# Kernel tuning notes

Hardware: AMD Instinct MI355X
Metric: run time of the kernel (lower is better)

The kernel has to match this reference:

```python
import jax, jax.numpy as jnp
import numpy as np

B = 8192         # graphs per batch
NPG = 39         # nodes per graph (from 4560 = 40*(105+9))
N = B * NPG      # total nodes
DEG = 8          # avg degree
E = N * DEG      # total edges
NEG_SLOPE = 0.2


def _glorot(key, shape):
    fan = sum(shape) if len(shape) > 1 else shape[0] + 1
    s = jnp.sqrt(6.0 / fan)
    return jax.random.uniform(key, shape, jnp.float32, -s, s)


def setup_inputs() -> dict:
    key = jax.random.key(0)
    ks = jax.random.split(key, 32)
    x = jax.random.normal(ks[0], (N, 1), jnp.float32)
    # edges constrained within each graph
    epg = NPG * DEG
    off = jnp.repeat(jnp.arange(B, dtype=jnp.int64) * NPG, epg)
    src = jax.random.randint(ks[1], (B * epg,), 0, NPG, jnp.int64) + off
    dst = jax.random.randint(ks[2], (B * epg,), 0, NPG, jnp.int64) + off
    edge_index = jnp.stack([src, dst], 0)
    batch_ids = jnp.repeat(jnp.arange(B, dtype=jnp.int64), NPG)
    dims = [(1, 8), (8, 64), (64, 32), (32, 9)]
    p = {}
    ki = 3
    for li, (fi, fo) in enumerate(dims, 1):
        p[f'W{li}'] = _glorot(ks[ki], (fi, fo)); ki += 1
        p[f'as{li}'] = _glorot(ks[ki], (fo,)); ki += 1
        p[f'ad{li}'] = _glorot(ks[ki], (fo,)); ki += 1
        p[f'b{li}'] = jnp.zeros((fo,), jnp.float32)
    p['lw1'] = _glorot(ks[ki], (4560, 1024)); ki += 1
    p['lb1'] = jnp.zeros((1024,), jnp.float32)
    p['lw2'] = _glorot(ks[ki], (1024, 128)); ki += 1
    p['lb2'] = jnp.zeros((128,), jnp.float32)
    p['lw3'] = _glorot(ks[ki], (128, 9)); ki += 1
    p['lb3'] = jnp.zeros((9,), jnp.float32)
    return {'x': x, 'edge_index': edge_index, 'batch_ids': batch_ids, **p}


def gat_layer(x, src, dst, W, a_s, a_d, b):
    # PyG GATConv, heads=1: h=xW; e_ij = LeakyReLU(a_s.h[src]+a_d.h[dst]);
    # softmax per destination node; out = sum_j alpha * h[src] + bias
    h = x @ W                                   # [N, Fo]
    s_n = h @ a_s                               # [N]
    d_n = h @ a_d                               # [N]
    e = jax.nn.leaky_relu(s_n[src] + d_n[dst], NEG_SLOPE)   # [E+N]
    m = jax.ops.segment_max(e, dst, num_segments=N)
    w = jnp.exp(e - m[dst])
    denom = jax.ops.segment_sum(w, dst, num_segments=N)
    alpha = w / (denom[dst] + 1e-16)
    out = jax.ops.segment_sum(h[src] * alpha[:, None], dst, num_segments=N)
    return out + b


def reference(x, edge_index, batch_ids, W1, as1, ad1, b1, W2, as2, ad2, b2,
              W3, as3, ad3, b3, W4, as4, ad4, b4, lw1, lb1, lw2, lb2, lw3, lb3):
    # add self-loops (PyG GATConv default)
    sl = jnp.arange(N, dtype=edge_index.dtype)
    src = jnp.concatenate([edge_index[0], sl])
    dst = jnp.concatenate([edge_index[1], sl])
    pool = lambda h: jax.ops.segment_max(h, batch_ids, num_segments=B)

    x0 = x.reshape(-1, 1)
    res = x0.reshape(B, -1)
    out0 = pool(x0)
    h1 = jax.nn.relu(gat_layer(x0, src, dst, W1, as1, ad1, b1))
    res1, out1 = h1.reshape(B, -1), pool(h1)
    h2 = jax.nn.relu(gat_layer(h1, src, dst, W2, as2, ad2, b2))
    res2, out2 = h2.reshape(B, -1), pool(h2)
    h3 = jax.nn.relu(gat_layer(h2, src, dst, W3, as3, ad3, b3))
    res3, out3 = h3.reshape(B, -1), pool(h3)
    h4 = jax.nn.relu(gat_layer(h3, src, dst, W4, as4, ad4, b4))
    res4, out4 = h4.reshape(B, -1), pool(h4)

    f = jnp.concatenate([res, res1, res2, res3, res4,
                         out0, out1, out2, out3, out4], axis=1)  # [B, 4560]
    f = jax.nn.relu(f @ lw1 + lb1)
    f = jax.nn.relu(f @ lw2 + lb2)
    return f @ lw3 + lb3
```

## Files before the change

kernel.cpp:

```cpp
#include <hip/hip_runtime.h>

#define NPG   39
#define NGRAPH 8192
#define EPG   312
#define EDG   351
#define E0    2555904
#define FDIM  4560
#define KP    4608

typedef __bf16 bf16x8 __attribute__((ext_vector_type(8)));
typedef float  f32x4  __attribute__((ext_vector_type(4)));

__device__ __forceinline__ unsigned short f2b(float f) {
  unsigned int u = __float_as_uint(f);
  u += 0x7fffu + ((u >> 16) & 1u);
  return (unsigned short)(u >> 16);
}
__device__ __forceinline__ unsigned int pk2(float lo, float hi) {
  return (unsigned int)f2b(lo) | ((unsigned int)f2b(hi) << 16);
}
__device__ __forceinline__ float b2f(unsigned short u) {
  return __uint_as_float((unsigned int)u << 16);
}
__device__ __forceinline__ void wsync() {
  asm volatile("s_waitcnt lgkmcnt(0)" ::: "memory");
}
__device__ __forceinline__ void gsync() {
  asm volatile("s_waitcnt vmcnt(0) lgkmcnt(0)" ::: "memory");
}

__shared__ alignas(16) unsigned short Htb[32 * 64];
__shared__ alignas(16) unsigned short alf16[40 * 64];
__shared__ float sn[40];
__shared__ float dn[48];
__shared__ unsigned char csr_src[EDG + 1];
__shared__ unsigned short csr_ptr[NPG + 1];

template<int Fi, int Fo, int KPAD, int KT1, int NT_STORE, int HALVES,
         int DT, int SCOL, int DCOL>
__device__ __forceinline__ void layerM(float x0,
                                       const unsigned short* __restrict__ Wb,
                                       const float* __restrict__ W1,
                                       const float* __restrict__ as1,
                                       const float* __restrict__ ad1,
                                       const float* __restrict__ bias,
                                       unsigned short* __restrict__ f_row,
                                       int in_off, int res_off, int out_off,
                                       int lane) {
  constexpr int NTH = NT_STORE / HALVES;
  const int r15 = lane & 15, g = lane >> 4;
  const f32x4 z = {0.f, 0.f, 0.f, 0.f};
  const uint4 z4 = {0u, 0u, 0u, 0u};

#pragma unroll
  for (int i = 0; i < 5; ++i) *(uint4*)&alf16[lane * 8 + i * 512] = z4;

  if constexpr (Fi == 1) {
    float was = 0.f, wad = 0.f;
#pragma unroll
    for (int o = 0; o < 8; ++o) { float w = W1[o]; was += w * as1[o]; wad += w * ad1[o]; }
    if (lane < NPG) {
      sn[lane] = x0 * was; dn[lane] = x0 * wad;
#pragma unroll
      for (int o = 0; o < 8; ++o) {
        int idx = o * 64 + ((((lane >> 3) ^ (o & 7)) << 3)) + (lane & 7);
        Htb[idx] = f2b(x0 * W1[o]);
      }
    }
  } else {
    gsync();
    f32x4 cd[3];
#pragma unroll
    for (int mt = 0; mt < 3; ++mt) cd[mt] = z;
#pragma unroll
    for (int kt = 0; kt < KT1; ++kt) {
      bf16x8 aF[3];
#pragma unroll
      for (int mt = 0; mt < 3; ++mt)
        aF[mt] = *(const bf16x8*)&f_row[in_off + (16 * mt + r15) * Fi + kt * 32 + g * 8];
      bf16x8 bD = *(const bf16x8*)&Wb[(16 * DT + r15) * KPAD + kt * 32 + g * 8];
#pragma unroll
      for (int mt = 0; mt < 3; ++mt)
        cd[mt] = __builtin_amdgcn_mfma_f32_16x16x32_bf16(aF[mt], bD, cd[mt], 0, 0, 0);
    }
#pragma unroll
    for (int mt = 0; mt < 3; ++mt)
#pragma unroll
      for (int v = 0; v < 4; ++v) {
        float t = cd[mt][v] + __shfl_xor(cd[mt][v], 4);
        int r = 16 * mt + g * 4 + v;
        if (r15 == SCOL && r < NPG) sn[r] = t;
        if (r15 == DCOL && r < NPG) dn[r] = t;
      }
  }
  wsync();

  if (lane < NPG) {
    int rs = csr_ptr[lane], re = csr_ptr[lane + 1];
    float dv = dn[lane];
    float m = -3.4e38f;
    for (int k = rs; k < re; ++k) {
      float e = sn[csr_src[k]] + dv;
      e = (e >= 0.f) ? e : 0.2f * e;
      m = fmaxf(m, e);
    }
    float den = 0.f;
    for (int k = rs; k < re; ++k) {
      int s = csr_src[k];
      float e = sn[s] + dv;
      e = (e >= 0.f) ? e : 0.2f * e;
      float w = __expf(e - m);
      int idx = lane * 64 + ((((s >> 3) ^ (lane & 7)) << 3)) + (s & 7);
      float cur = b2f(alf16[idx]);
      unsigned short nb = f2b(cur + w);
      alf16[idx] = nb;
      den += b2f(nb) - cur;
    }
    dn[lane] = 1.f / (den + 1e-16f);
  }
  wsync();

  float invr[3][4];
#pragma unroll
  for (int mt = 0; mt < 3; ++mt)
#pragma unroll
    for (int v = 0; v < 4; ++v) invr[mt][v] = dn[16 * mt + g * 4 + v];

  float pool_[NT_STORE];
#pragma unroll
  for (int s = 0; s < NT_STORE; ++s) pool_[s] = 0.f;

#pragma unroll
  for (int h = 0; h < HALVES; ++h) {
    if constexpr (Fi > 1) {
      f32x4 c1[3][NTH];
#pragma unroll
      for (int mt = 0; mt < 3; ++mt)
#pragma unroll
        for (int tl = 0; tl < NTH; ++tl) c1[mt][tl] = z;
#pragma unroll
      for (int kt = 0; kt < KT1; ++kt) {
        bf16x8 aF[3];
#pragma unroll
        for (int mt = 0; mt < 3; ++mt)
          aF[mt] = *(const bf16x8*)&f_row[in_off + (16 * mt + r15) * Fi + kt * 32 + g * 8];
#pragma unroll
        for (int tl = 0; tl < NTH; ++tl) {
          int nt = h * NTH + tl;
          bf16x8 bW = *(const bf16x8*)&Wb[(16 * nt + r15) * KPAD + kt * 32 + g * 8];
#pragma unroll
          for (int mt = 0; mt < 3; ++mt)
            c1[mt][tl] = __builtin_amdgcn_mfma_f32_16x16x32_bf16(aF[mt], bW, c1[mt][tl], 0, 0, 0);
        }
      }
#pragma unroll
      for (int tl = 0; tl < NTH; ++tl) {
        int p = r15 + 16 * tl;
#pragma unroll
        for (int mt = 0; mt < 3; ++mt) {
          uint2 w;
          w.x = pk2(c1[mt][tl][0], c1[mt][tl][1]);
          w.y = pk2(c1[mt][tl][2], c1[mt][tl][3]);
          int idx = p * 64 + (((2 * mt + (g >> 1)) ^ (p & 7)) << 3) + (g & 1) * 4;
          *(uint2*)&Htb[idx] = w;
        }
      }
    }
    wsync();
    f32x4 c2[3][NTH];
#pragma unroll
    for (int mt = 0; mt < 3; ++mt)
#pragma unroll
      for (int tl = 0; tl < NTH; ++tl) c2[mt][tl] = z;
#pragma unroll
    for (int kt = 0; kt < 2; ++kt) {
      bf16x8 aA[3];
#pragma unroll
      for (int mt = 0; mt < 3; ++mt) {
        int row = 16 * mt + r15;
        aA[mt] = *(const bf16x8*)&alf16[row * 64 + ((((4 * kt + g) ^ (row & 7))) << 3)];
      }
#pragma unroll
      for (int tl = 0; tl < NTH; ++tl) {
        int p = r15 + 16 * tl;
        bf16x8 bH = *(const bf16x8*)&Htb[p * 64 + ((((4 * kt + g) ^ (p & 7))) << 3)];
#pragma unroll
        for (int mt = 0; mt < 3; ++mt)
          c2[mt][tl] = __builtin_amdgcn_mfma_f32_16x16x32_bf16(aA[mt], bH, c2[mt][tl], 0, 0, 0);
      }
    }
#pragma unroll
    for (int tl = 0; tl < NTH; ++tl) {
      int c = r15 + 16 * (h * NTH + tl);
      float bv = (c < Fo) ? bias[c] : 0.f;
#pragma unroll
      for (int mt = 0; mt < 3; ++mt)
#pragma unroll
        for (int v = 0; v < 4; ++v) {
          int r = 16 * mt + g * 4 + v;
          float val = fmaxf(c2[mt][tl][v] * invr[mt][v] + bv, 0.f);
          if (r < NPG && c < Fo) {
            f_row[res_off + r * Fo + c] = f2b(val);
            pool_[h * NTH + tl] = fmaxf(pool_[h * NTH + tl], val);
          }
        }
    }
    wsync();
  }

#pragma unroll
  for (int s = 0; s < NT_STORE; ++s) {
    float pv = pool_[s];
    pv = fmaxf(pv, __shfl_xor(pv, 16));
    pv = fmaxf(pv, __shfl_xor(pv, 32));
    int c = r15 + 16 * s;
    if (g == 0 && c < Fo) f_row[out_off + c] = f2b(pv);
  }
}

__global__ __launch_bounds__(64, 4) void gat_fused(
    const float* __restrict__ x, const int* __restrict__ ei,
    const float* __restrict__ W1, const float* __restrict__ as1, const float* __restrict__ ad1,
    const float* __restrict__ b1, const float* __restrict__ b2,
    const float* __restrict__ b3, const float* __restrict__ b4,
    const unsigned short* __restrict__ Wb,
    unsigned short* __restrict__ f) {
  const int b = blockIdx.x;
  const int lane = threadIdx.x;
  const int base = b * NPG;
  const int* srcg = ei + (size_t)b * EPG;
  const int* dstg = ei + E0 + (size_t)b * EPG;
  unsigned short* f_row = f + (size_t)b * KP;
  int* cnt = (int*)sn;
  const uint4 z4 = {0u, 0u, 0u, 0u};

#pragma unroll
  for (int i = 0; i < 4; ++i) *(uint4*)&Htb[lane * 8 + i * 512] = z4;

  float xv = 0.f;
  if (lane < NPG) {
    xv = x[(size_t)base + lane];
    f_row[lane] = f2b(xv);
  }
  if (lane == 0) f_row[39] = 0;
  if (lane < KP - 4561) f_row[4561 + lane] = 0;
  float mx = (lane < NPG) ? xv : -3.4e38f;
#pragma unroll
  for (int st = 1; st < 64; st <<= 1) { float t = __shfl_xor(mx, st); mx = fmaxf(mx, t); }
  if (lane == 0) f_row[4447] = f2b(mx);
  if (lane < NPG) cnt[lane] = 1;
  wsync();

  int es[5], ed[5];
#pragma unroll
  for (int it = 0; it < 5; ++it) {
    int e = lane + 64 * it;
    if (e < EPG) {
      int s = srcg[e] - base, d = dstg[e] - base;
      s = min(max(s, 0), NPG - 1);
      d = min(max(d, 0), NPG - 1);
      es[it] = s; ed[it] = d;
      atomicAdd(&cnt[d], 1);
    } else { es[it] = -1; ed[it] = 0; }
  }
  wsync();

  int c = (lane < NPG) ? cnt[lane] : 0;
  int v = c;
#pragma unroll
  for (int off = 1; off < 64; off <<= 1) { int t = __shfl_up(v, off); if (lane >= off) v += t; }
  int excl = v - c;
  if (lane < NPG) csr_ptr[lane] = (unsigned short)excl;
  if (lane == NPG - 1) csr_ptr[NPG] = (unsigned short)EDG;
  wsync();
  if (lane < NPG) cnt[lane] = excl;
  wsync();

  if (lane < NPG) { int p = atomicAdd(&cnt[lane], 1); csr_src[p] = (unsigned char)lane; }
#pragma unroll
  for (int it = 0; it < 5; ++it) {
    if (es[it] >= 0) {
      int p = atomicAdd(&cnt[ed[it]], 1);
      p = min(p, EDG - 1);
      csr_src[p] = (unsigned char)es[it];
    }
  }
  wsync();

  const unsigned short* Wb2 = Wb;
  const unsigned short* Wb3 = Wb + 2560;
  const unsigned short* Wb4 = Wb + 5632;

  layerM< 1,  8,  0,  0,  1,  1,  0,  0,  0>(xv, nullptr, W1, as1, ad1, b1, f_row, 0,    40,   4448, lane);
  layerM< 8, 64, 32,  1,  4,  2,  4,  0,  1>(0.f, Wb2, nullptr, nullptr, nullptr, b2, f_row, 40,   352,  4456, lane);
  layerM<64, 32, 64,  2,  2,  1,  2,  0,  1>(0.f, Wb3, nullptr, nullptr, nullptr, b3, f_row, 352,  2848, 4520, lane);
  layerM<32,  9, 32,  1,  1,  1,  0, 10, 11>(0.f, Wb4, nullptr, nullptr, nullptr, b4, f_row, 2848, 4096, 4552, lane);
}

__global__ __launch_bounds__(256) void prep_wb(
    const float* __restrict__ W2, const float* __restrict__ as2, const float* __restrict__ ad2,
    const float* __restrict__ W3, const float* __restrict__ as3, const float* __restrict__ ad3,
    const float* __restrict__ W4, const float* __restrict__ as4, const float* __restrict__ ad4,
    unsigned short* __restrict__ Wb) {
  const int tid = threadIdx.x;
  for (int i = tid; i < 80 * 32; i += 256) {
    int o = i >> 5, k = i & 31; float v = 0.f;
    if (k < 8) {
      if (o < 64) v = W2[k * 64 + o];
      else if (o == 64 || o == 68) { float s = 0; for (int j = 0; j < 64; ++j) s += W2[k * 64 + j] * as2[j];
        float hi = b2f(f2b(s)); v = (o == 64) ? hi : (s - hi); }
      else if (o == 65 || o == 69) { float s = 0; for (int j = 0; j < 64; ++j) s += W2[k * 64 + j] * ad2[j];
        float hi = b2f(f2b(s)); v = (o == 65) ? hi : (s - hi); }
    }
    Wb[i] = f2b(v);
  }
  for (int i = tid; i < 48 * 64; i += 256) {
    int o = i >> 6, k = i & 63; float v = 0.f;
    if (o < 32) v = W3[k * 32 + o];
    else if (o == 32 || o == 36) { float s = 0; for (int j = 0; j < 32; ++j) s += W3[k * 32 + j] * as3[j];
      float hi = b2f(f2b(s)); v = (o == 32) ? hi : (s - hi); }
    else if (o == 33 || o == 37) { float s = 0; for (int j = 0; j < 32; ++j) s += W3[k * 32 + j] * ad3[j];
      float hi = b2f(f2b(s)); v = (o == 33) ? hi : (s - hi); }
    Wb[2560 + i] = f2b(v);
  }
  for (int i = tid; i < 16 * 32; i += 256) {
    int o = i >> 5, k = i & 31; float v = 0.f;
    if (o < 9) v = W4[k * 9 + o];
    else if (o == 10 || o == 14) { float s = 0; for (int j = 0; j < 9; ++j) s += W4[k * 9 + j] * as4[j];
      float hi = b2f(f2b(s)); v = (o == 10) ? hi : (s - hi); }
    else if (o == 11 || o == 15) { float s = 0; for (int j = 0; j < 9; ++j) s += W4[k * 9 + j] * ad4[j];
      float hi = b2f(f2b(s)); v = (o == 11) ? hi : (s - hi); }
    Wb[5632 + i] = f2b(v);
  }
}

template<bool PERM>
__global__ __launch_bounds__(256) void tcast(const float* __restrict__ in,
                                             unsigned short* __restrict__ out,
                                             int K, int NN, int Kpad) {
  __shared__ float tile[64 * 65];
  const int k0 = blockIdx.x * 64, n0 = blockIdx.y * 64;
  const int tid = threadIdx.x;
#pragma unroll
  for (int i = 0; i < 16; ++i) {
    int idx = i * 256 + tid;
    int r = idx >> 6, c = idx & 63;
    int k = k0 + r;
    int ko;
    if constexpr (PERM) {
      ko = (k < 39) ? k : ((k == 39 || k > FDIM) ? -1 : k - 1);
    } else {
      ko = (k < K) ? k : -1;
    }
    tile[r * 65 + c] = (ko >= 0) ? in[(size_t)ko * NN + n0 + c] : 0.f;
  }
  __syncthreads();
#pragma unroll
  for (int i = 0; i < 16; ++i) {
    int idx = i * 256 + tid;
    int r = idx >> 6, c = idx & 63;
    out[(size_t)(n0 + r) * Kpad + k0 + c] = f2b(tile[c * 65 + r]);
  }
}

template<bool OUT_BF16>
__global__ __launch_bounds__(256) void mfma_gemm(const unsigned short* __restrict__ A,
    const unsigned short* __restrict__ Bt, unsigned short* __restrict__ Cb,
    float* __restrict__ Cf, const float* __restrict__ bias, int K, int N, int gridN) {
  __shared__ alignas(16) unsigned short As[128 * 64];
  __shared__ alignas(16) unsigned short Bs[128 * 64];
  const int tid = threadIdx.x;
  const int lane = tid & 63;
  const int wave = tid >> 6;
  const int wy = wave >> 1, wx = wave & 1;

  const int wg = blockIdx.x;
  const int xcd = wg & 7, idx = wg >> 3;
  const int mpr = (int)(gridDim.x >> 3) / gridN;
  const int m_local = idx / gridN;
  const int n = idx - m_local * gridN;
  const int m0 = (xcd * mpr + m_local) * 128;
  const int n0 = n * 128;

  f32x4 acc[4][4];
  const f32x4 z = {0.f, 0.f, 0.f, 0.f};
#pragma unroll
  for (int i = 0; i < 4; ++i)
#pragma unroll
    for (int j = 0; j < 4; ++j) acc[i][j] = z;

  const int srow = lane >> 3;
  const int sch  = (lane & 7) ^ srow;
  const int q    = lane >> 4;
  const int rm   = lane & 15;

  for (int k0 = 0; k0 < K; k0 += 64) {
    __syncthreads();
#pragma unroll
    for (int t = 0; t < 4; ++t) {
      int r0 = wave * 32 + t * 8;
      const unsigned short* ga = A  + (size_t)(m0 + r0 + srow) * K + k0 + sch * 8;
      const unsigned short* gb = Bt + (size_t)(n0 + r0 + srow) * K + k0 + sch * 8;
      __builtin_amdgcn_global_load_lds(
          (const __attribute__((address_space(1))) unsigned int*)(const void*)ga,
          (__attribute__((address_space(3))) unsigned int*)(void*)&As[r0 * 64], 16, 0, 0);
      __builtin_amdgcn_global_load_lds(
          (const __attribute__((address_space(1))) unsigned int*)(const void*)gb,
          (__attribute__((address_space(3))) unsigned int*)(void*)&Bs[r0 * 64], 16, 0, 0);
    }
    __syncthreads();
#pragma unroll
    for (int kk = 0; kk < 2; ++kk) {
      bf16x8 af[4], bfr[4];
#pragma unroll
      for (int i = 0; i < 4; ++i) {
        int ra = wy * 64 + i * 16 + rm;
        int rb = wx * 64 + i * 16 + rm;
        af[i]  = *(const bf16x8*)&As[ra * 64 + (((kk * 4 + q) ^ (ra & 7)) << 3)];
        bfr[i] = *(const bf16x8*)&Bs[rb * 64 + (((kk * 4 + q) ^ (rb & 7)) << 3)];
      }
#pragma unroll
      for (int i = 0; i < 4; ++i)
#pragma unroll
        for (int j = 0; j < 4; ++j)
          acc[i][j] = __builtin_amdgcn_mfma_f32_16x16x32_bf16(af[i], bfr[j], acc[i][j], 0, 0, 0);
    }
  }
  const int q4 = (lane >> 4) * 4;
#pragma unroll
  for (int i = 0; i < 4; ++i) {
#pragma unroll
    for (int j = 0; j < 4; ++j) {
      int row = m0 + wy * 64 + i * 16 + q4;
      int col = n0 + wx * 64 + j * 16 + rm;
      float bv = bias[col];
#pragma unroll
      for (int v = 0; v < 4; ++v) {
        float val = fmaxf(acc[i][j][v] + bv, 0.f);
        if constexpr (OUT_BF16) Cb[(size_t)(row + v) * N + col] = f2b(val);
        else                    Cf[(size_t)(row + v) * N + col] = val;
      }
    }
  }
}

__global__ __launch_bounds__(256) void mlp3(const float* __restrict__ g2,
                                            const float* __restrict__ w3,
                                            const float* __restrict__ b3,
                                            float* __restrict__ out) {
  __shared__ float gs[64 * 130];
  __shared__ float ws3[128 * 9];
  const int r0 = blockIdx.x * 64;
  const int tid = threadIdx.x;
  for (int i = tid; i < 64 * 128; i += 256)
    gs[(i >> 7) * 130 + (i & 127)] = g2[(size_t)r0 * 128 + i];
  for (int i = tid; i < 128 * 9; i += 256) ws3[i] = w3[i];
  __syncthreads();
  for (int idx = tid; idx < 64 * 9; idx += 256) {
    int r = idx / 9, c = idx - r * 9;
    float acc = b3[c];
#pragma unroll 8
    for (int k = 0; k < 128; ++k) acc += gs[r * 130 + k] * ws3[k * 9 + c];
    out[(size_t)(r0 + r) * 9 + c] = acc;
  }
}

extern "C" void kernel_launch(void* const* d_in, const int* in_sizes, int n_in,
                              void* d_out, int out_size, void* d_ws, size_t ws_size,
                              hipStream_t stream) {
  const float* x   = (const float*)d_in[0];
  const int*   ei  = (const int*)d_in[1];
  const float* W1  = (const float*)d_in[3];
  const float* as1 = (const float*)d_in[4];
  const float* ad1 = (const float*)d_in[5];
  const float* b1  = (const float*)d_in[6];
  const float* W2  = (const float*)d_in[7];
  const float* as2 = (const float*)d_in[8];
  const float* ad2 = (const float*)d_in[9];
  const float* b2  = (const float*)d_in[10];
  const float* W3  = (const float*)d_in[11];
  const float* as3 = (const float*)d_in[12];
  const float* ad3 = (const float*)d_in[13];
  const float* b3  = (const float*)d_in[14];
  const float* W4  = (const float*)d_in[15];
  const float* as4 = (const float*)d_in[16];
  const float* ad4 = (const float*)d_in[17];
  const float* b4  = (const float*)d_in[18];
  const float* lw1 = (const float*)d_in[19];
  const float* lb1 = (const float*)d_in[20];
  const float* lw2 = (const float*)d_in[21];
  const float* lb2 = (const float*)d_in[22];
  const float* lw3 = (const float*)d_in[23];
  const float* lb3 = (const float*)d_in[24];
  float* out = (float*)d_out;

  unsigned short* f   = (unsigned short*)d_ws;
  unsigned short* w1t = f   + (size_t)NGRAPH * KP;
  unsigned short* w2t = w1t + (size_t)1024 * KP;
  unsigned short* g1  = w2t + (size_t)128 * 1024;
  float*          g2  = (float*)(g1 + (size_t)NGRAPH * 1024);
  unsigned short* Wb  = g1;

  prep_wb<<<1, 256, 0, stream>>>(W2, as2, ad2, W3, as3, ad3, W4, as4, ad4, Wb);
  tcast<true ><<<dim3(KP / 64, 1024 / 64), 256, 0, stream>>>(lw1, w1t, FDIM, 1024, KP);
  tcast<false><<<dim3(1024 / 64, 128 / 64), 256, 0, stream>>>(lw2, w2t, 1024, 128, 1024);

  gat_fused<<<NGRAPH, 64, 0, stream>>>(x, ei, W1, as1, ad1,
      b1, b2, b3, b4, Wb, f);

  mfma_gemm<true ><<<512, 256, 0, stream>>>(
      f, w1t, g1, nullptr, lb1, KP, 1024, 8);
  mfma_gemm<false><<<64, 256, 0, stream>>>(
      g1, w2t, nullptr, g2, lb2, 1024, 128, 1);

  mlp3<<<NGRAPH / 64, 256, 0, stream>>>(g2, lw3, lb3, out);
}
```

Before: 225.9 us.

## Stage inter-layer activations in swizzled LDS and write rows with vector stores

Each GAT layer now writes its activations to a swizzled shared-memory buffer (Xin for 8-wide, Abuf16a otherwise), and the next layer reads its MFMA operands from LDS instead of reloading them from the global feature row. The global stores become coalesced 16-byte copies, and the vmcnt wait before each layer is removed. This takes the global write-then-read round trip off the critical path. The extra LDS buffers raise per-block shared memory, so the launch bound occupancy hint drops from 4 to 2 blocks.

```diff
diff --git a/kernel.cpp b/kernel.cpp
--- a/kernel.cpp
+++ b/kernel.cpp
@@ -25,12 +25,11 @@
 __device__ __forceinline__ void wsync() {
   asm volatile("s_waitcnt lgkmcnt(0)" ::: "memory");
 }
-__device__ __forceinline__ void gsync() {
-  asm volatile("s_waitcnt vmcnt(0) lgkmcnt(0)" ::: "memory");
-}
 
 __shared__ alignas(16) unsigned short Htb[32 * 64];
 __shared__ alignas(16) unsigned short alf16[40 * 64];
+__shared__ alignas(16) unsigned short Abuf16a[40 * 64];
+__shared__ alignas(16) unsigned short Xin[416];
 __shared__ float sn[40];
 __shared__ float dn[48];
 __shared__ unsigned char csr_src[EDG + 1];
@@ -45,13 +44,19 @@
                                        const float* __restrict__ ad1,
                                        const float* __restrict__ bias,
                                        unsigned short* __restrict__ f_row,
-                                       int in_off, int res_off, int out_off,
-                                       int lane) {
+                                       int res_off, int out_off, int lane) {
   constexpr int NTH = NT_STORE / HALVES;
+  constexpr int RMASK = (Fi >= 16) ? (Fi / 8 - 1) : 0;
+  constexpr int WMASK = (Fo >= 16) ? (Fo / 8 - 1) : 0;
+  constexpr bool INX  = (Fi == 8);
+  constexpr bool OUTX = (Fo == 8);
   const int r15 = lane & 15, g = lane >> 4;
   const f32x4 z = {0.f, 0.f, 0.f, 0.f};
   const uint4 z4 = {0u, 0u, 0u, 0u};
 
+  const unsigned short* inb = INX ? Xin : Abuf16a;
+  unsigned short* outb = OUTX ? Xin : Abuf16a;
+
 #pragma unroll
   for (int i = 0; i < 5; ++i) *(uint4*)&alf16[lane * 8 + i * 512] = z4;
 
@@ -68,7 +73,6 @@
       }
     }
   } else {
-    gsync();
     f32x4 cd[3];
 #pragma unroll
     for (int mt = 0; mt < 3; ++mt) cd[mt] = z;
@@ -76,8 +80,11 @@
     for (int kt = 0; kt < KT1; ++kt) {
       bf16x8 aF[3];
 #pragma unroll
-      for (int mt = 0; mt < 3; ++mt)
-        aF[mt] = *(const bf16x8*)&f_row[in_off + (16 * mt + r15) * Fi + kt * 32 + g * 8];
+      for (int mt = 0; mt < 3; ++mt) {
+        int row = 16 * mt + r15;
+        if constexpr (Fi == 64) row = (row > 39) ? 39 : row;
+        aF[mt] = *(const bf16x8*)&inb[row * Fi + (((kt * 4 + g) ^ (row & RMASK)) << 3)];
+      }
       bf16x8 bD = *(const bf16x8*)&Wb[(16 * DT + r15) * KPAD + kt * 32 + g * 8];
 #pragma unroll
       for (int mt = 0; mt < 3; ++mt)
@@ -142,8 +149,11 @@
       for (int kt = 0; kt < KT1; ++kt) {
         bf16x8 aF[3];
 #pragma unroll
-        for (int mt = 0; mt < 3; ++mt)
-          aF[mt] = *(const bf16x8*)&f_row[in_off + (16 * mt + r15) * Fi + kt * 32 + g * 8];
+        for (int mt = 0; mt < 3; ++mt) {
+          int row = 16 * mt + r15;
+          if constexpr (Fi == 64) row = (row > 39) ? 39 : row;
+          aF[mt] = *(const bf16x8*)&inb[row * Fi + (((kt * 4 + g) ^ (row & RMASK)) << 3)];
+        }
 #pragma unroll
         for (int tl = 0; tl < NTH; ++tl) {
           int nt = h * NTH + tl;
@@ -200,12 +210,30 @@
           int r = 16 * mt + g * 4 + v;
           float val = fmaxf(c2[mt][tl][v] * invr[mt][v] + bv, 0.f);
           if (r < NPG && c < Fo) {
-            f_row[res_off + r * Fo + c] = f2b(val);
+            outb[r * Fo + ((((c >> 3) ^ (r & WMASK)) << 3) | (c & 7))] = f2b(val);
             pool_[h * NTH + tl] = fmaxf(pool_[h * NTH + tl], val);
           }
         }
     }
     wsync();
+  }
+
+  constexpr int TOT  = NPG * Fo;
+  constexpr int OCTS = TOT / 8;
+  constexpr int OPRo = Fo / 8;
+  for (int j = lane; j < OCTS; j += 64) {
+    uint4 w;
+    if constexpr (WMASK > 0) {
+      int r = j / OPRo, o = j - r * OPRo;
+      w = *(const uint4*)&outb[r * Fo + ((o ^ (r & WMASK)) << 3)];
+    } else {
+      w = *(const uint4*)&outb[j * 8];
+    }
+    *(uint4*)&f_row[res_off + j * 8] = w;
+  }
+  if constexpr ((TOT % 8) != 0) {
+    if (lane < (TOT % 8))
+      f_row[res_off + OCTS * 8 + lane] = outb[OCTS * 8 + lane];
   }
 
 #pragma unroll
@@ -218,7 +246,7 @@
   }
 }
 
-__global__ __launch_bounds__(64, 4) void gat_fused(
+__global__ __launch_bounds__(64, 2) void gat_fused(
     const float* __restrict__ x, const int* __restrict__ ei,
     const float* __restrict__ W1, const float* __restrict__ as1, const float* __restrict__ ad1,
     const float* __restrict__ b1, const float* __restrict__ b2,
@@ -236,6 +264,9 @@
 
 #pragma unroll
   for (int i = 0; i < 4; ++i) *(uint4*)&Htb[lane * 8 + i * 512] = z4;
+#pragma unroll
+  for (int i = 0; i < 5; ++i) *(uint4*)&Abuf16a[lane * 8 + i * 512] = z4;
+  if (lane < 52) *(uint4*)&Xin[lane * 8] = z4;
 
   float xv = 0.f;
   if (lane < NPG) {
@@ -291,10 +322,10 @@
   const unsigned short* Wb3 = Wb + 2560;
   const unsigned short* Wb4 = Wb + 5632;
 
-  layerM< 1,  8,  0,  0,  1,  1,  0,  0,  0>(xv, nullptr, W1, as1, ad1, b1, f_row, 0,    40,   4448, lane);
-  layerM< 8, 64, 32,  1,  4,  2,  4,  0,  1>(0.f, Wb2, nullptr, nullptr, nullptr, b2, f_row, 40,   352,  4456, lane);
-  layerM<64, 32, 64,  2,  2,  1,  2,  0,  1>(0.f, Wb3, nullptr, nullptr, nullptr, b3, f_row, 352,  2848, 4520, lane);
-  layerM<32,  9, 32,  1,  1,  1,  0, 10, 11>(0.f, Wb4, nullptr, nullptr, nullptr, b4, f_row, 2848, 4096, 4552, lane);
+  layerM< 1,  8,  0,  0,  1,  1,  0,  0,  0>(xv, nullptr, W1, as1, ad1, b1, f_row, 40,   4448, lane);
+  layerM< 8, 64, 32,  1,  4,  2,  4,  0,  1>(0.f, Wb2, nullptr, nullptr, nullptr, b2, f_row, 352,  4456, lane);
+  layerM<64, 32, 64,  2,  2,  1,  2,  0,  1>(0.f, Wb3, nullptr, nullptr, nullptr, b3, f_row, 2848, 4520, lane);
+  layerM<32,  9, 32,  1,  1,  1,  0, 10, 11>(0.f, Wb4, nullptr, nullptr, nullptr, b4, f_row, 4096, 4552, lane);
 }
 
 __global__ __launch_bounds__(256) void prep_wb(
```

Result: slower. 257.1 us (+13.8%).
